# Kernel optimization log

Measured on AMD Instinct MI355X. Metric: run time of the kernel, lower is better.

The kernel has to match this reference:

```python
import math
import jax, jax.numpy as jnp
import numpy as np

THETA = 2 ** 16

def _get_freqs(n: int) -> jnp.ndarray:
    # positions quantized to multiples of 2 (pairs share a frequency)
    pos = jnp.floor(jnp.arange(n, dtype=jnp.float32) / 2.0) * 2.0
    return 1.0 / (THETA ** (pos / n)) / (2.0 * math.pi)  # (n,)

def _rope(phases: jnp.ndarray, v: jnp.ndarray) -> jnp.ndarray:
    # phases in 'cycles'; wrap to [0,1) then scale to radians
    ph = (phases % 1.0) * (2.0 * math.pi)
    c, s = jnp.cos(ph), jnp.sin(ph)
    # interleaved rotate-half: out[..., 2i] = -v[..., 2i+1], out[..., 2i+1] = v[..., 2i]
    v_rot = jnp.stack((-v[..., 1::2], v[..., ::2]), axis=-1).reshape(v.shape)
    return (v * c).astype(v.dtype) + (v_rot * s).astype(v.dtype)


def setup_inputs() -> dict:
    key = jax.random.key(0)
    kq, kv = jax.random.split(key)
    B, H, T, N, D = 2, 8, 2048, 1024, 128
    Q = jax.random.normal(kq, (B, H, T, N), dtype=jnp.float32)
    K = Q  # module asserts K is Q
    V = jax.random.normal(kv, (B, H, T, D), dtype=jnp.float32)
    return {"Q": Q, "K": K, "V": V}


def reference(Q, K, V):
    B, H, T, N = Q.shape
    freqs = _get_freqs(N)  # (N,)
    # r_phases: (T, N) = position * freq (broadcast over B, H)
    r_phases = jnp.arange(T, dtype=jnp.float32)[:, None] * freqs[None, :]
    QR = _rope(r_phases, Q)  # (B,H,T,N); KR = QR since K is Q
    scores = jnp.einsum('bhtn,bhsn->bhts', QR, QR)  # (B,H,T,T)
    causal = jnp.tril(jnp.ones((T, T), dtype=bool), k=-1)  # strict lower triangle
    scores = jnp.where(causal, scores, 0.0)
    return jnp.einsum('bhts,bhsd->bhtd', scores, V)  # (B,H,T,D)
```

## Files before the change

kernel.cpp:

```cpp
#include <hip/hip_runtime.h>

typedef __bf16 bf16_t;
typedef bf16_t bf16x8 __attribute__((ext_vector_type(8)));
typedef float f32x4 __attribute__((ext_vector_type(4)));
typedef unsigned short u16;
typedef unsigned int u32;

#define T_DIM 2048
#define N_DIM 1024
#define D_DIM 128

__device__ __forceinline__ u16 f32_to_bf16(float f) {
    u32 u = __builtin_bit_cast(u32, f);
    u += 0x7FFFu + ((u >> 16) & 1u);
    return (u16)(u >> 16);
}
__device__ __forceinline__ float bf16_to_f32(u16 v) {
    u32 u = (u32)v << 16;
    return __builtin_bit_cast(float, u);
}

typedef __attribute__((address_space(1))) const u32 guint;
typedef __attribute__((address_space(3))) u32 luint;
__device__ __forceinline__ void stage16(const void* g, void* l) {
    __builtin_amdgcn_global_load_lds((guint*)g, (luint*)l, 16, 0, 0);
}

__global__ void rope_kernel(const float* __restrict__ Q, u16* __restrict__ QR) {
    const int g = blockIdx.x * 256 + threadIdx.x;
    const int base = g * 4;
    const int t  = (base >> 9) & (T_DIM - 1);
    const int p0 = base & 511;
    const float4 qa = ((const float4*)Q)[g * 2];
    const float4 qb = ((const float4*)Q)[g * 2 + 1];
    const float vin[4][2] = {{qa.x, qa.y}, {qa.z, qa.w}, {qb.x, qb.y}, {qb.z, qb.w}};
    u16 ov[8];
    #pragma unroll
    for (int uu = 0; uu < 4; ++uu) {
        const float freq = exp2f((float)(p0 + uu) * (-1.0f / 32.0f)) * 0.15915494309189535f;
        float ph = (float)t * freq;
        ph = ph - floorf(ph);
        const float s = __builtin_amdgcn_sinf(ph);
        const float c = __builtin_amdgcn_cosf(ph);
        ov[2 * uu]     = f32_to_bf16(vin[uu][0] * c - vin[uu][1] * s);
        ov[2 * uu + 1] = f32_to_bf16(vin[uu][1] * c + vin[uu][0] * s);
    }
    ((uint4*)QR)[g] = *(const uint4*)ov;
}

__global__ void vt_kernel(const float* __restrict__ V, u16* __restrict__ Vt) {
    __shared__ u16 tile[64][65];
    const int bh   = blockIdx.x >> 6;
    const int rem  = blockIdx.x & 63;
    const int t0 = (rem >> 1) * 64, d0 = (rem & 1) * 64;
    const float* src = V + ((size_t)bh * T_DIM + t0) * D_DIM + d0;
    #pragma unroll
    for (int k = 0; k < 16; ++k) {
        int linear = k * 256 + threadIdx.x;
        int r = linear >> 6, c = linear & 63;
        tile[r][c] = f32_to_bf16(src[(size_t)r * D_DIM + c]);
    }
    __syncthreads();
    u16* dst = Vt + ((size_t)bh * D_DIM + d0) * T_DIM + t0;
    #pragma unroll
    for (int k = 0; k < 16; ++k) {
        int linear = k * 256 + threadIdx.x;
        int dr = linear >> 6, tc = linear & 63;
        dst[(size_t)dr * T_DIM + tc] = tile[tc][dr];
    }
}

__global__ void qrt_kernel(const u16* __restrict__ QR, u16* __restrict__ QRt) {
    __shared__ u16 til[64][65];
    const int bh  = blockIdx.x >> 9;
    const int rem = blockIdx.x & 511;
    const int t0 = (rem >> 4) * 64, n0 = (rem & 15) * 64;
    const u16* src = QR + (size_t)bh * ((size_t)T_DIM * N_DIM) + (size_t)t0 * N_DIM + n0;
    #pragma unroll
    for (int k = 0; k < 2; ++k) {
        int linear = k * 256 + threadIdx.x;
        int r = linear >> 3, o = linear & 7;
        uint4 v = *(const uint4*)(src + (size_t)r * N_DIM + o * 8);
        u16 tmp[8]; *(uint4*)tmp = v;
        #pragma unroll
        for (int e = 0; e < 8; ++e) til[r][o * 8 + e] = tmp[e];
    }
    __syncthreads();
    u16* dst = QRt + (size_t)bh * ((size_t)N_DIM * T_DIM) + (size_t)n0 * T_DIM + t0;
    #pragma unroll
    for (int k = 0; k < 2; ++k) {
        int linear = k * 256 + threadIdx.x;
        int nl = linear >> 3, to = linear & 7;
        u16 tmp[8];
        #pragma unroll
        for (int e = 0; e < 8; ++e) tmp[e] = til[to * 8 + e][nl];
        *(uint4*)(dst + (size_t)nl * T_DIM + to * 8) = *(const uint4*)tmp;
    }
}

__global__ __launch_bounds__(256, 2)
void state_kernel(const u16* __restrict__ QRt, const u16* __restrict__ Vt,
                  u16* __restrict__ U) {
    __shared__ __align__(16) u16 Smem[16384];
    u16 (*As)[64] = (u16 (*)[64])Smem;
    u16 (*Bs)[64] = (u16 (*)[64])(Smem + 8192);

    const int ci = blockIdx.x >> 3;
    const int nt = blockIdx.x & 7;
    const int bh = ci >> 4;
    const int i  = ci & 15;

    const int tid  = threadIdx.x;
    const int w    = tid >> 6;
    const int wy   = w >> 1, wx = w & 1;
    const int lane = tid & 63;
    const int quad = lane >> 4;
    const int l15  = lane & 15;
    const int sw   = l15 & 7;
    const int srow = lane >> 3;
    const int scol = (lane & 7) ^ (srow & 7);

    const u16* Ap = Vt + (size_t)bh * ((size_t)D_DIM * T_DIM)
                       + (size_t)(w * 32 + srow) * T_DIM + i * 128 + scol * 8;
    const u16* Bp = QRt + (size_t)bh * ((size_t)N_DIM * T_DIM)
                        + (size_t)(nt * 128 + w * 32 + srow) * T_DIM + i * 128 + scol * 8;

    const f32x4 fz = {0.f, 0.f, 0.f, 0.f};
    f32x4 acc[4][4];
    #pragma unroll
    for (int mi = 0; mi < 4; ++mi)
        #pragma unroll
        for (int nj = 0; nj < 4; ++nj)
            acc[mi][nj] = fz;

    for (int kk = 0; kk < 128; kk += 64) {
        #pragma unroll
        for (int ii = 0; ii < 4; ++ii) {
            stage16(Ap + (size_t)ii * 8 * T_DIM + kk, &As[w * 32 + ii * 8][0]);
            stage16(Bp + (size_t)ii * 8 * T_DIM + kk, &Bs[w * 32 + ii * 8][0]);
        }
        __syncthreads();
        #pragma unroll
        for (int kc = 0; kc < 2; ++kc) {
            bf16x8 af[4], bfr[4];
            #pragma unroll
            for (int mi = 0; mi < 4; ++mi)
                af[mi] = *(const bf16x8*)((const char*)As + (wy * 64 + mi * 16 + l15) * 128 + (((kc * 4 + quad) ^ sw) << 4));
            #pragma unroll
            for (int nj = 0; nj < 4; ++nj)
                bfr[nj] = *(const bf16x8*)((const char*)Bs + (wx * 64 + nj * 16 + l15) * 128 + (((kc * 4 + quad) ^ sw) << 4));
            #pragma unroll
            for (int mi = 0; mi < 4; ++mi)
                #pragma unroll
                for (int nj = 0; nj < 4; ++nj)
                    acc[mi][nj] = __builtin_amdgcn_mfma_f32_16x16x32_bf16(af[mi], bfr[nj], acc[mi][nj], 0, 0, 0);
        }
        __syncthreads();
    }

    u16* ub = U + (size_t)ci * (128 * (size_t)N_DIM) + nt * 128;
    #pragma unroll
    for (int mi = 0; mi < 4; ++mi)
        #pragma unroll
        for (int nj = 0; nj < 4; ++nj)
            #pragma unroll
            for (int rr = 0; rr < 4; ++rr)
                ub[(size_t)(wy * 64 + mi * 16 + quad * 4 + rr) * N_DIM + wx * 64 + nj * 16 + l15]
                    = f32_to_bf16(acc[mi][nj][rr]);
}

__global__ void scan_kernel(u16* __restrict__ UP) {
    const int tg  = blockIdx.x * 256 + threadIdx.x;
    const int bh  = tg >> 14;
    const int rem = tg & 16383;
    u16* base = UP + ((size_t)bh * 16 * 128 + (rem >> 7)) * N_DIM + (size_t)(rem & 127) * 8;
    float s[8];
    #pragma unroll
    for (int e = 0; e < 8; ++e) s[e] = 0.f;
    #pragma unroll 1
    for (int i = 0; i < 16; ++i) {
        u16* p = base + (size_t)i * (128 * (size_t)N_DIM);
        uint4 v = *(const uint4*)p;
        u16 in[8]; *(uint4*)in = v;
        u16 out[8];
        #pragma unroll
        for (int e = 0; e < 8; ++e) {
            float f = bf16_to_f32(in[e]);
            out[e]  = f32_to_bf16(s[e]);
            s[e]   += f;
        }
        *(uint4*)p = *(const uint4*)out;
    }
}

__global__ __launch_bounds__(256, 2)
void attn2_kernel(const u16* __restrict__ QR, const u16* __restrict__ Pt,
                  const u16* __restrict__ Vt, float* __restrict__ Out,
                  float* __restrict__ Part) {
    __shared__ __align__(16) u16 Smem[17920];
    u16 (*As)[64]  = (u16 (*)[64])Smem;
    u16 (*Bs)[64]  = (u16 (*)[64])(Smem + 8192);
    u16 (*Ps)[140] = (u16 (*)[140])Smem;

    const int b = blockIdx.x;
    const bool is_main = b < 256;
    const int ci = is_main ? b : b - 256;
    const int bh = ci >> 4;
    const int i  = ci & 15;

    const int tid  = threadIdx.x;
    const int w    = tid >> 6;
    const int wy   = w >> 1, wx = w & 1;
    const int lane = tid & 63;
    const int quad = lane >> 4;
    const int l15  = lane & 15;
    const int sw   = l15 & 7;
    const int srow = lane >> 3;
    const int scol = (lane & 7) ^ (srow & 7);

    const u16* QRb = QR + (size_t)bh * ((size_t)T_DIM * N_DIM);
    const u16* Ap  = QRb + (size_t)(i * 128 + w * 32 + srow) * N_DIM + scol * 8;
    const u16* Bp  = is_main
        ? Pt + (size_t)(ci * 128 + w * 32 + srow) * N_DIM + scol * 8
        : Ap;

    const f32x4 fz = {0.f, 0.f, 0.f, 0.f};
    f32x4 s_acc[4][4];
    #pragma unroll
    for (int mi = 0; mi < 4; ++mi)
        #pragma unroll
        for (int nj = 0; nj < 4; ++nj)
            s_acc[mi][nj] = fz;

    for (int kk = 0; kk < N_DIM; kk += 64) {
        #pragma unroll
        for (int ii = 0; ii < 4; ++ii) {
            stage16(Ap + (size_t)ii * 8 * N_DIM + kk, &As[w * 32 + ii * 8][0]);
            stage16(Bp + (size_t)ii * 8 * N_DIM + kk, &Bs[w * 32 + ii * 8][0]);
        }
        __syncthreads();
        #pragma unroll
        for (int kc = 0; kc < 2; ++kc) {
            bf16x8 af[4], bfr[4];
            #pragma unroll
            for (int mi = 0; mi < 4; ++mi)
                af[mi] = *(const bf16x8*)((const char*)As + (wy * 64 + mi * 16 + l15) * 128 + (((kc * 4 + quad) ^ sw) << 4));
            #pragma unroll
            for (int nj = 0; nj < 4; ++nj)
                bfr[nj] = *(const bf16x8*)((const char*)Bs + (wx * 64 + nj * 16 + l15) * 128 + (((kc * 4 + quad) ^ sw) << 4));
            #pragma unroll
            for (int mi = 0; mi < 4; ++mi)
                #pragma unroll
                for (int nj = 0; nj < 4; ++nj)
                    s_acc[mi][nj] = __builtin_amdgcn_mfma_f32_16x16x32_bf16(af[mi], bfr[nj], s_acc[mi][nj], 0, 0, 0);
        }
        __syncthreads();
    }

    if (is_main) {
        float* pb = Part + (size_t)ci * 16384;
        #pragma unroll
        for (int mi = 0; mi < 4; ++mi)
            #pragma unroll
            for (int nj = 0; nj < 4; ++nj)
                #pragma unroll
                for (int rr = 0; rr < 4; ++rr)
                    pb[(wy * 64 + mi * 16 + quad * 4 + rr) * 128 + wx * 64 + nj * 16 + l15]
                        = s_acc[mi][nj][rr];
    } else {
        #pragma unroll
        for (int mi = 0; mi < 4; ++mi) {
            const int rowb = wy * 64 + mi * 16 + quad * 4;
            #pragma unroll
            for (int nj = 0; nj < 4; ++nj) {
                const int col = wx * 64 + nj * 16 + l15;
                #pragma unroll
                for (int rr = 0; rr < 4; ++rr)
                    if (col >= rowb + rr) s_acc[mi][nj][rr] = 0.f;
            }
        }
        #pragma unroll
        for (int mi = 0; mi < 4; ++mi) {
            const int rowb = wy * 64 + mi * 16 + quad * 4;
            #pragma unroll
            for (int nj = 0; nj < 4; ++nj) {
                const int col = wx * 64 + nj * 16 + l15;
                #pragma unroll
                for (int rr = 0; rr < 4; ++rr)
                    Ps[rowb + rr][col] = f32_to_bf16(s_acc[mi][nj][rr]);
            }
        }
        __syncthreads();

        f32x4 o_acc[4][4];
        #pragma unroll
        for (int mi = 0; mi < 4; ++mi)
            #pragma unroll
            for (int nj = 0; nj < 4; ++nj)
                o_acc[mi][nj] = fz;

        const u16* vjb = Vt + (size_t)bh * ((size_t)D_DIM * T_DIM)
                            + (size_t)(wx * 64 + l15) * T_DIM + i * 128 + quad * 8;
        #pragma unroll
        for (int kc = 0; kc < 4; ++kc) {
            bf16x8 pf[4];
            #pragma unroll
            for (int mi = 0; mi < 4; ++mi)
                pf[mi] = *(const bf16x8*)(&Ps[wy * 64 + mi * 16 + l15][kc * 32 + quad * 8]);
            #pragma unroll
            for (int nj = 0; nj < 4; ++nj) {
                const bf16x8 vv = *(const bf16x8*)(vjb + (size_t)(nj * 16) * T_DIM + kc * 32);
                #pragma unroll
                for (int mi = 0; mi < 4; ++mi)
                    o_acc[mi][nj] = __builtin_amdgcn_mfma_f32_16x16x32_bf16(pf[mi], vv, o_acc[mi][nj], 0, 0, 0);
            }
        }

        float* ob = Out + ((size_t)bh * T_DIM + (size_t)i * 128) * D_DIM;
        #pragma unroll
        for (int mi = 0; mi < 4; ++mi)
            #pragma unroll
            for (int nj = 0; nj < 4; ++nj)
                #pragma unroll
                for (int rr = 0; rr < 4; ++rr)
                    ob[(size_t)(wy * 64 + mi * 16 + quad * 4 + rr) * D_DIM + wx * 64 + nj * 16 + l15]
                        = o_acc[mi][nj][rr];
    }
}

__global__ void combine2_kernel(float* __restrict__ Out, const float* __restrict__ Part) {
    const int idx = blockIdx.x * 256 + threadIdx.x;
    float4 a = ((float4*)Out)[idx];
    const float4 p = ((const float4*)Part)[idx];
    a.x += p.x; a.y += p.y; a.z += p.z; a.w += p.w;
    ((float4*)Out)[idx] = a;
}

__device__ __forceinline__ int run_start(int b) { return b < 128 ? 5 * b : 640 + 4 * (b - 128); }

__global__ __launch_bounds__(256, 2)
void attn_kernel(const u16* __restrict__ QR, const u16* __restrict__ Vt,
                 float* __restrict__ Out, u16* __restrict__ Part) {
    __shared__ __align__(16) u16 Smem[17920];
    u16 (*As)[64]  = (u16 (*)[64])Smem;
    u16 (*Bs)[64]  = (u16 (*)[64])(Smem + 8192);
    u16 (*Ps)[140] = (u16 (*)[140])Smem;

    const int b     = blockIdx.x;
    const int start = run_start(b);
    const int len   = b < 128 ? 5 : 4;

    const int tid  = threadIdx.x;
    const int w    = tid >> 6;
    const int wy   = w >> 1, wx = w & 1;
    const int lane = tid & 63;
    const int quad = lane >> 4;
    const int l15  = lane & 15;
    const int sw   = l15 & 7;
    const int srow = lane >> 3;
    const int scol = (lane & 7) ^ (srow & 7);

    const f32x4 fz = {0.f, 0.f, 0.f, 0.f};
    f32x4 o_acc[4][4];
    int cur_bh = -1, cur_qt = -1;
    bool hasj0 = false;
    const u16* QRb = QR;
    const u16* Ap  = QR;
    const u16* Vb  = Vt;

    for (int it = 0; it < len; ++it) {
        const int i = start + it;
        const int bh = i / 136;
        const int r  = i - bh * 136;
        int qt = 15, j = 0, acc = 0;
        #pragma unroll 1
        for (int q = 0; q < 16; ++q) {
            if (r < acc + q + 1) { qt = q; j = r - acc; break; }
            acc += q + 1;
        }

        if (qt != cur_qt || bh != cur_bh) {
            if (cur_qt >= 0) {
                if (hasj0) {
                    float* ob = Out + ((size_t)cur_bh * T_DIM + (size_t)cur_qt * 128) * D_DIM;
                    #pragma unroll
                    for (int mi = 0; mi < 4; ++mi)
                        #pragma unroll
                        for (int nj = 0; nj < 4; ++nj)
                            #pragma unroll
                            for (int rr = 0; rr < 4; ++rr)
                                ob[(size_t)(wy * 64 + mi * 16 + quad * 4 + rr) * D_DIM + wx * 64 + nj * 16 + l15] = o_acc[mi][nj][rr];
                } else {
                    u16* pb = Part + (size_t)b * 16384;
                    #pragma unroll
                    for (int mi = 0; mi < 4; ++mi)
                        #pragma unroll
                        for (int nj = 0; nj < 4; ++nj)
                            #pragma unroll
                            for (int rr = 0; rr < 4; ++rr)
                                pb[(wy * 64 + mi * 16 + quad * 4 + rr) * 128 + wx * 64 + nj * 16 + l15] = f32_to_bf16(o_acc[mi][nj][rr]);
                }
            }
            cur_bh = bh; cur_qt = qt; hasj0 = (j == 0);
            #pragma unroll
            for (int mi = 0; mi < 4; ++mi)
                #pragma unroll
                for (int nj = 0; nj < 4; ++nj)
                    o_acc[mi][nj] = fz;
            QRb = QR + (size_t)bh * (T_DIM * N_DIM);
            Ap  = QRb + (size_t)(qt * 128 + w * 32 + srow) * N_DIM + scol * 8;
            Vb  = Vt + (size_t)bh * (D_DIM * T_DIM) + (size_t)(wx * 64 + l15) * T_DIM + quad * 8;
        }

        const u16* Bp = QRb + (size_t)(j * 128 + w * 32 + srow) * N_DIM + scol * 8;
        f32x4 s_acc[4][4];
        #pragma unroll
        for (int mi = 0; mi < 4; ++mi)
            #pragma unroll
            for (int nj = 0; nj < 4; ++nj)
                s_acc[mi][nj] = fz;

        __syncthreads();

        for (int kk = 0; kk < N_DIM; kk += 64) {
            #pragma unroll
            for (int ii = 0; ii < 4; ++ii) {
                stage16(Ap + (size_t)ii * 8 * N_DIM + kk, &As[w * 32 + ii * 8][0]);
                stage16(Bp + (size_t)ii * 8 * N_DIM + kk, &Bs[w * 32 + ii * 8][0]);
            }
            __syncthreads();
            #pragma unroll
            for (int kc = 0; kc < 2; ++kc) {
                bf16x8 af[4], bfr[4];
                #pragma unroll
                for (int mi = 0; mi < 4; ++mi)
                    af[mi] = *(const bf16x8*)((const char*)As + (wy * 64 + mi * 16 + l15) * 128 + (((kc * 4 + quad) ^ sw) << 4));
                #pragma unroll
                for (int nj = 0; nj < 4; ++nj)
                    bfr[nj] = *(const bf16x8*)((const char*)Bs + (wx * 64 + nj * 16 + l15) * 128 + (((kc * 4 + quad) ^ sw) << 4));
                #pragma unroll
                for (int mi = 0; mi < 4; ++mi)
                    #pragma unroll
                    for (int nj = 0; nj < 4; ++nj)
                        s_acc[mi][nj] = __builtin_amdgcn_mfma_f32_16x16x32_bf16(af[mi], bfr[nj], s_acc[mi][nj], 0, 0, 0);
            }
            __syncthreads();
        }

        if (j == qt) {
            #pragma unroll
            for (int mi = 0; mi < 4; ++mi) {
                const int rowb = wy * 64 + mi * 16 + quad * 4;
                #pragma unroll
                for (int nj = 0; nj < 4; ++nj) {
                    const int col = wx * 64 + nj * 16 + l15;
                    #pragma unroll
                    for (int rr = 0; rr < 4; ++rr)
                        if (col >= rowb + rr) s_acc[mi][nj][rr] = 0.f;
                }
            }
        }

        #pragma unroll
        for (int mi = 0; mi < 4; ++mi) {
            const int rowb = wy * 64 + mi * 16 + quad * 4;
            #pragma unroll
            for (int nj = 0; nj < 4; ++nj) {
                const int col = wx * 64 + nj * 16 + l15;
                #pragma unroll
                for (int rr = 0; rr < 4; ++rr)
                    Ps[rowb + rr][col] = f32_to_bf16(s_acc[mi][nj][rr]);
            }
        }
        __syncthreads();

        const u16* vjb = Vb + j * 128;
        #pragma unroll
        for (int kc = 0; kc < 4; ++kc) {
            bf16x8 pf[4];
            #pragma unroll
            for (int mi = 0; mi < 4; ++mi)
                pf[mi] = *(const bf16x8*)(&Ps[wy * 64 + mi * 16 + l15][kc * 32 + quad * 8]);
            #pragma unroll
            for (int nj = 0; nj < 4; ++nj) {
                const bf16x8 vv = *(const bf16x8*)(vjb + (size_t)(nj * 16) * T_DIM + kc * 32);
                #pragma unroll
                for (int mi = 0; mi < 4; ++mi)
                    o_acc[mi][nj] = __builtin_amdgcn_mfma_f32_16x16x32_bf16(pf[mi], vv, o_acc[mi][nj], 0, 0, 0);
            }
        }
    }

    if (hasj0) {
        float* ob = Out + ((size_t)cur_bh * T_DIM + (size_t)cur_qt * 128) * D_DIM;
        #pragma unroll
        for (int mi = 0; mi < 4; ++mi)
            #pragma unroll
            for (int nj = 0; nj < 4; ++nj)
                #pragma unroll
                for (int rr = 0; rr < 4; ++rr)
                    ob[(size_t)(wy * 64 + mi * 16 + quad * 4 + rr) * D_DIM + wx * 64 + nj * 16 + l15] = o_acc[mi][nj][rr];
    } else {
        u16* pb = Part + (size_t)b * 16384;
        #pragma unroll
        for (int mi = 0; mi < 4; ++mi)
            #pragma unroll
            for (int nj = 0; nj < 4; ++nj)
                #pragma unroll
                for (int rr = 0; rr < 4; ++rr)
                    pb[(wy * 64 + mi * 16 + quad * 4 + rr) * 128 + wx * 64 + nj * 16 + l15] = f32_to_bf16(o_acc[mi][nj][rr]);
    }
}

__global__ void combine_kernel(float* __restrict__ Out, const u16* __restrict__ Part) {
    const int bh = blockIdx.x & 15;
    const int qt = 1 + (blockIdx.x >> 4);
    const int ts = bh * 136 + (qt * (qt + 1)) / 2;
    const int lo = ts + 1, hi = ts + qt;
    int bmin = (lo <= 640) ? (lo + 4) / 5 : 128 + (lo - 640 + 3) / 4;
    int writers[4], nw = 0;
    for (int bb = bmin; bb < 512 && run_start(bb) <= hi && nw < 4; ++bb)
        writers[nw++] = bb;
    if (nw == 0) return;
    float* ob = Out + ((size_t)bh * T_DIM + (size_t)qt * 128) * D_DIM;
    const int tid = threadIdx.x;
    #pragma unroll 1
    for (int e = 0; e < 64; ++e) {
        const int idx = e * 256 + tid;
        float a = ob[idx];
        for (int k = 0; k < nw; ++k)
            a += bf16_to_f32(Part[(size_t)writers[k] * 16384 + idx]);
        ob[idx] = a;
    }
}

extern "C" void kernel_launch(void* const* d_in, const int* in_sizes, int n_in,
                              void* d_out, int out_size, void* d_ws, size_t ws_size,
                              hipStream_t stream) {
    const float* Q = (const float*)d_in[0];
    const float* V = (const float*)d_in[2];
    float* Out = (float*)d_out;

    const size_t QR_E = (size_t)16 * T_DIM * N_DIM;
    const size_t VT_E = (size_t)16 * D_DIM * T_DIM;
    const size_t P_E  = (size_t)256 * 128 * N_DIM;
    const size_t need = (QR_E * 2 + VT_E + P_E) * 2 + (size_t)256 * 16384 * 4;

    if (ws_size >= need) {
        u16* QRw  = (u16*)d_ws;
        u16* QRtw = QRw + QR_E;
        u16* Vtw  = QRtw + QR_E;
        u16* Ptw  = Vtw + VT_E;
        float* PartF = (float*)(Ptw + P_E);

        rope_kernel<<<dim3(16384), dim3(256), 0, stream>>>(Q, QRw);
        vt_kernel<<<dim3(1024), dim3(256), 0, stream>>>(V, Vtw);
        qrt_kernel<<<dim3(8192), dim3(256), 0, stream>>>(QRw, QRtw);
        state_kernel<<<dim3(2048), dim3(256), 0, stream>>>(QRtw, Vtw, Ptw);
        scan_kernel<<<dim3(1024), dim3(256), 0, stream>>>(Ptw);
        attn2_kernel<<<dim3(512), dim3(256), 0, stream>>>(QRw, Ptw, Vtw, Out, PartF);
        combine2_kernel<<<dim3(4096), dim3(256), 0, stream>>>(Out, PartF);
    } else {
        u16* QRw  = (u16*)d_ws;
        u16* Vtw  = QRw + QR_E;
        u16* Part = Vtw + VT_E;

        rope_kernel<<<dim3(16384), dim3(256), 0, stream>>>(Q, QRw);
        vt_kernel<<<dim3(1024), dim3(256), 0, stream>>>(V, Vtw);
        attn_kernel<<<dim3(512), dim3(256), 0, stream>>>(QRw, Vtw, Out, Part);
        combine_kernel<<<dim3(240), dim3(256), 0, stream>>>(Out, Part);
    }
}
```

Before: 373.9 us.

## Fuse rope with transpose, state with scan, and merge attention blocks

Rope and the QR transpose now happen in one kernel, which removes a full re-read of QR. The per-chunk state GEMM and the prefix scan become one kernel that keeps a running fp32 accumulator across T chunks with double-buffered LDS staging, so the separate scan pass and its read-modify-write are gone. The inter-chunk and intra-chunk score GEMMs are merged into one attention kernel that shares A tiles and adds the intra result into the same accumulator, which eliminates combine2 and the fp32 partial buffer. The cost is fewer blocks (256) at occupancy 1, and the serial state kernel runs a 30-step loop, which can hurt parallelism on a GPU with many CUs.

```diff
diff --git a/kernel.cpp b/kernel.cpp
--- a/kernel.cpp
+++ b/kernel.cpp
@@ -24,6 +24,290 @@
 typedef __attribute__((address_space(3))) u32 luint;
 __device__ __forceinline__ void stage16(const void* g, void* l) {
     __builtin_amdgcn_global_load_lds((guint*)g, (luint*)l, 16, 0, 0);
+}
+__device__ __forceinline__ void wait_vm0_barrier() {
+    asm volatile("s_waitcnt vmcnt(0)" ::: "memory");
+    __builtin_amdgcn_s_barrier();
+}
+
+__global__ void ropet_kernel(const float* __restrict__ Q, u16* __restrict__ QR,
+                             u16* __restrict__ QRt) {
+    __shared__ u16 til[64][65];
+    const int bh  = blockIdx.x >> 9;
+    const int rem = blockIdx.x & 511;
+    const int t0 = (rem >> 4) * 64, n0 = (rem & 15) * 64;
+    const float* src = Q + (size_t)bh * ((size_t)T_DIM * N_DIM) + (size_t)t0 * N_DIM + n0;
+    u16* qdst = QR + (size_t)bh * ((size_t)T_DIM * N_DIM) + (size_t)t0 * N_DIM + n0;
+    #pragma unroll
+    for (int k = 0; k < 4; ++k) {
+        const int linear = k * 256 + threadIdx.x;
+        const int r = linear >> 4;
+        const int f = linear & 15;
+        const float4 q = *(const float4*)(src + (size_t)r * N_DIM + f * 4);
+        const int t = t0 + r;
+        u16 o[4];
+        #pragma unroll
+        for (int pp = 0; pp < 2; ++pp) {
+            const int pidx = ((n0 + f * 4) >> 1) + pp;
+            const float freq = exp2f((float)pidx * (-1.0f / 32.0f)) * 0.15915494309189535f;
+            float ph = (float)t * freq;
+            ph -= floorf(ph);
+            const float s = __builtin_amdgcn_sinf(ph);
+            const float c = __builtin_amdgcn_cosf(ph);
+            const float a  = pp ? q.z : q.x;
+            const float b2 = pp ? q.w : q.y;
+            o[2 * pp]     = f32_to_bf16(a * c - b2 * s);
+            o[2 * pp + 1] = f32_to_bf16(b2 * c + a * s);
+        }
+        *(uint2*)(qdst + (size_t)r * N_DIM + f * 4) = *(const uint2*)o;
+        til[r][f * 4 + 0] = o[0]; til[r][f * 4 + 1] = o[1];
+        til[r][f * 4 + 2] = o[2]; til[r][f * 4 + 3] = o[3];
+    }
+    __syncthreads();
+    u16* tdst = QRt + (size_t)bh * ((size_t)N_DIM * T_DIM) + (size_t)n0 * T_DIM + t0;
+    #pragma unroll
+    for (int k = 0; k < 2; ++k) {
+        const int linear = k * 256 + threadIdx.x;
+        const int nl = linear >> 3, o = linear & 7;
+        u16 tmp[8];
+        #pragma unroll
+        for (int e = 0; e < 8; ++e) tmp[e] = til[o * 8 + e][nl];
+        *(uint4*)(tdst + (size_t)nl * T_DIM + o * 8) = *(const uint4*)tmp;
+    }
+}
+
+__global__ void vt_kernel(const float* __restrict__ V, u16* __restrict__ Vt) {
+    __shared__ u16 tile[64][65];
+    const int bh   = blockIdx.x >> 6;
+    const int rem  = blockIdx.x & 63;
+    const int t0 = (rem >> 1) * 64, d0 = (rem & 1) * 64;
+    const float* src = V + ((size_t)bh * T_DIM + t0) * D_DIM + d0;
+    #pragma unroll
+    for (int k = 0; k < 16; ++k) {
+        int linear = k * 256 + threadIdx.x;
+        int r = linear >> 6, c = linear & 63;
+        tile[r][c] = f32_to_bf16(src[(size_t)r * D_DIM + c]);
+    }
+    __syncthreads();
+    u16* dst = Vt + ((size_t)bh * D_DIM + d0) * T_DIM + t0;
+    #pragma unroll
+    for (int k = 0; k < 16; ++k) {
+        int linear = k * 256 + threadIdx.x;
+        int dr = linear >> 6, tc = linear & 63;
+        dst[(size_t)dr * T_DIM + tc] = tile[tc][dr];
+    }
+}
+
+__global__ __launch_bounds__(256, 1)
+void statescan_kernel(const u16* __restrict__ QRt, const u16* __restrict__ Vt,
+                      u16* __restrict__ UP) {
+    __shared__ __align__(16) u16 Smem[24576];
+
+    const int b  = blockIdx.x;
+    const int bh = b >> 4;
+    const int nt = (b >> 1) & 7;
+    const int dt = b & 1;
+
+    const int tid  = threadIdx.x;
+    const int w    = tid >> 6;
+    const int wy   = w >> 1, wx = w & 1;
+    const int lane = tid & 63;
+    const int quad = lane >> 4;
+    const int l15  = lane & 15;
+    const int sw   = l15 & 7;
+    const int srow = lane >> 3;
+    const int scol = (lane & 7) ^ (srow & 7);
+
+    const u16* Ag = Vt  + (size_t)bh * ((size_t)D_DIM * T_DIM) + (size_t)(dt * 64)  * T_DIM;
+    const u16* Bg = QRt + (size_t)bh * ((size_t)N_DIM * T_DIM) + (size_t)(nt * 128) * T_DIM;
+
+    const f32x4 fz = {0.f, 0.f, 0.f, 0.f};
+    f32x4 acc[2][4];
+    #pragma unroll
+    for (int mi = 0; mi < 2; ++mi)
+        #pragma unroll
+        for (int nj = 0; nj < 4; ++nj)
+            acc[mi][nj] = fz;
+
+    auto STAGE = [&](int buf, int s) {
+        const int toff = s * 64;
+        #pragma unroll
+        for (int ia = 0; ia < 2; ++ia)
+            stage16(Ag + (size_t)(w * 16 + ia * 8 + srow) * T_DIM + toff + scol * 8,
+                    Smem + buf * 4096 + (w * 16 + ia * 8) * 64);
+        #pragma unroll
+        for (int ib = 0; ib < 4; ++ib)
+            stage16(Bg + (size_t)(w * 32 + ib * 8 + srow) * T_DIM + toff + scol * 8,
+                    Smem + 8192 + buf * 8192 + (w * 32 + ib * 8) * 64);
+    };
+
+    u16* upb = UP + (size_t)(bh * 16) * (128 * (size_t)N_DIM)
+                  + (size_t)(dt * 64) * N_DIM + nt * 128;
+
+    auto WRITE_UP = [&](int ci) {
+        u16* ub = upb + (size_t)ci * (128 * (size_t)N_DIM);
+        #pragma unroll
+        for (int mi = 0; mi < 2; ++mi)
+            #pragma unroll
+            for (int nj = 0; nj < 4; ++nj)
+                #pragma unroll
+                for (int rr = 0; rr < 4; ++rr)
+                    ub[(size_t)(wy * 32 + mi * 16 + quad * 4 + rr) * N_DIM + wx * 64 + nj * 16 + l15]
+                        = f32_to_bf16(acc[mi][nj][rr]);
+    };
+
+    STAGE(0, 0);
+    wait_vm0_barrier();
+    int buf = 0;
+    for (int s = 0; s < 30; ++s) {
+        if ((s & 1) == 0) WRITE_UP(s >> 1);
+        if (s < 29) STAGE(buf ^ 1, s + 1);
+        const char* As = (const char*)(Smem + buf * 4096);
+        const char* Bs = (const char*)(Smem + 8192 + buf * 8192);
+        #pragma unroll
+        for (int kc = 0; kc < 2; ++kc) {
+            bf16x8 af[2], bfr[4];
+            #pragma unroll
+            for (int mi = 0; mi < 2; ++mi)
+                af[mi] = *(const bf16x8*)(As + (wy * 32 + mi * 16 + l15) * 128 + (((kc * 4 + quad) ^ sw) << 4));
+            #pragma unroll
+            for (int nj = 0; nj < 4; ++nj)
+                bfr[nj] = *(const bf16x8*)(Bs + (wx * 64 + nj * 16 + l15) * 128 + (((kc * 4 + quad) ^ sw) << 4));
+            #pragma unroll
+            for (int mi = 0; mi < 2; ++mi)
+                #pragma unroll
+                for (int nj = 0; nj < 4; ++nj)
+                    acc[mi][nj] = __builtin_amdgcn_mfma_f32_16x16x32_bf16(af[mi], bfr[nj], acc[mi][nj], 0, 0, 0);
+        }
+        wait_vm0_barrier();
+        buf ^= 1;
+    }
+    WRITE_UP(15);
+}
+
+__global__ __launch_bounds__(256, 1)
+void attn3_kernel(const u16* __restrict__ QR, const u16* __restrict__ UP,
+                  const u16* __restrict__ Vt, float* __restrict__ Out) {
+    __shared__ __align__(16) u16 Smem[32768];
+    u16 (*Ps)[140] = (u16 (*)[140])Smem;
+
+    const int b  = blockIdx.x;
+    const int bh = b >> 4;
+    const int i  = b & 15;
+
+    const int tid  = threadIdx.x;
+    const int w    = tid >> 6;
+    const int wy   = w >> 1, wx = w & 1;
+    const int lane = tid & 63;
+    const int quad = lane >> 4;
+    const int l15  = lane & 15;
+    const int sw   = l15 & 7;
+    const int srow = lane >> 3;
+    const int scol = (lane & 7) ^ (srow & 7);
+
+    const u16* Ap = QR + (size_t)bh * ((size_t)T_DIM * N_DIM)
+                       + (size_t)(i * 128 + w * 32 + srow) * N_DIM + scol * 8;
+    const u16* Bp = UP + (size_t)(b * 128 + w * 32 + srow) * N_DIM + scol * 8;
+
+    const f32x4 fz = {0.f, 0.f, 0.f, 0.f};
+    f32x4 sm[4][4], si[4][4];
+    #pragma unroll
+    for (int mi = 0; mi < 4; ++mi)
+        #pragma unroll
+        for (int nj = 0; nj < 4; ++nj) {
+            sm[mi][nj] = fz;
+            si[mi][nj] = fz;
+        }
+
+    auto STAGE = [&](int buf, int kk16) {
+        const int kk = kk16 * 64;
+        #pragma unroll
+        for (int ii = 0; ii < 4; ++ii) {
+            stage16(Ap + (size_t)(ii * 8) * N_DIM + kk, Smem + buf * 8192 + (w * 32 + ii * 8) * 64);
+            stage16(Bp + (size_t)(ii * 8) * N_DIM + kk, Smem + 16384 + buf * 8192 + (w * 32 + ii * 8) * 64);
+        }
+    };
+
+    STAGE(0, 0);
+    wait_vm0_barrier();
+    int buf = 0;
+    for (int kk16 = 0; kk16 < 16; ++kk16) {
+        if (kk16 < 15) STAGE(buf ^ 1, kk16 + 1);
+        const char* As = (const char*)(Smem + buf * 8192);
+        const char* Bs = (const char*)(Smem + 16384 + buf * 8192);
+        #pragma unroll
+        for (int kc = 0; kc < 2; ++kc) {
+            bf16x8 af[4], bm[4], bi[4];
+            #pragma unroll
+            for (int mi = 0; mi < 4; ++mi)
+                af[mi] = *(const bf16x8*)(As + (wy * 64 + mi * 16 + l15) * 128 + (((kc * 4 + quad) ^ sw) << 4));
+            #pragma unroll
+            for (int nj = 0; nj < 4; ++nj) {
+                bm[nj] = *(const bf16x8*)(Bs + (wx * 64 + nj * 16 + l15) * 128 + (((kc * 4 + quad) ^ sw) << 4));
+                bi[nj] = *(const bf16x8*)(As + (wx * 64 + nj * 16 + l15) * 128 + (((kc * 4 + quad) ^ sw) << 4));
+            }
+            #pragma unroll
+            for (int mi = 0; mi < 4; ++mi)
+                #pragma unroll
+                for (int nj = 0; nj < 4; ++nj) {
+                    sm[mi][nj] = __builtin_amdgcn_mfma_f32_16x16x32_bf16(af[mi], bm[nj], sm[mi][nj], 0, 0, 0);
+                    si[mi][nj] = __builtin_amdgcn_mfma_f32_16x16x32_bf16(af[mi], bi[nj], si[mi][nj], 0, 0, 0);
+                }
+        }
+        wait_vm0_barrier();
+        buf ^= 1;
+    }
+
+    #pragma unroll
+    for (int mi = 0; mi < 4; ++mi) {
+        const int rowb = wy * 64 + mi * 16 + quad * 4;
+        #pragma unroll
+        for (int nj = 0; nj < 4; ++nj) {
+            const int col = wx * 64 + nj * 16 + l15;
+            #pragma unroll
+            for (int rr = 0; rr < 4; ++rr)
+                if (col >= rowb + rr) si[mi][nj][rr] = 0.f;
+        }
+    }
+    #pragma unroll
+    for (int mi = 0; mi < 4; ++mi) {
+        const int rowb = wy * 64 + mi * 16 + quad * 4;
+        #pragma unroll
+        for (int nj = 0; nj < 4; ++nj) {
+            const int col = wx * 64 + nj * 16 + l15;
+            #pragma unroll
+            for (int rr = 0; rr < 4; ++rr)
+                Ps[rowb + rr][col] = f32_to_bf16(si[mi][nj][rr]);
+        }
+    }
+    __syncthreads();
+
+    const u16* vjb = Vt + (size_t)bh * ((size_t)D_DIM * T_DIM)
+                        + (size_t)(wx * 64 + l15) * T_DIM + i * 128 + quad * 8;
+    #pragma unroll
+    for (int kc = 0; kc < 4; ++kc) {
+        bf16x8 pf[4];
+        #pragma unroll
+        for (int mi = 0; mi < 4; ++mi)
+            pf[mi] = *(const bf16x8*)(&Ps[wy * 64 + mi * 16 + l15][kc * 32 + quad * 8]);
+        #pragma unroll
+        for (int nj = 0; nj < 4; ++nj) {
+            const bf16x8 vv = *(const bf16x8*)(vjb + (size_t)(nj * 16) * T_DIM + kc * 32);
+            #pragma unroll
+            for (int mi = 0; mi < 4; ++mi)
+                sm[mi][nj] = __builtin_amdgcn_mfma_f32_16x16x32_bf16(pf[mi], vv, sm[mi][nj], 0, 0, 0);
+        }
+    }
+
+    float* ob = Out + ((size_t)bh * T_DIM + (size_t)i * 128) * D_DIM;
+    #pragma unroll
+    for (int mi = 0; mi < 4; ++mi)
+        #pragma unroll
+        for (int nj = 0; nj < 4; ++nj)
+            #pragma unroll
+            for (int rr = 0; rr < 4; ++rr)
+                ob[(size_t)(wy * 64 + mi * 16 + quad * 4 + rr) * D_DIM + wx * 64 + nj * 16 + l15]
+                    = sm[mi][nj][rr];
 }
 
 __global__ void rope_kernel(const float* __restrict__ Q, u16* __restrict__ QR) {
@@ -46,294 +330,6 @@
         ov[2 * uu + 1] = f32_to_bf16(vin[uu][1] * c + vin[uu][0] * s);
     }
     ((uint4*)QR)[g] = *(const uint4*)ov;
-}
-
-__global__ void vt_kernel(const float* __restrict__ V, u16* __restrict__ Vt) {
-    __shared__ u16 tile[64][65];
-    const int bh   = blockIdx.x >> 6;
-    const int rem  = blockIdx.x & 63;
-    const int t0 = (rem >> 1) * 64, d0 = (rem & 1) * 64;
-    const float* src = V + ((size_t)bh * T_DIM + t0) * D_DIM + d0;
-    #pragma unroll
-    for (int k = 0; k < 16; ++k) {
-        int linear = k * 256 + threadIdx.x;
-        int r = linear >> 6, c = linear & 63;
-        tile[r][c] = f32_to_bf16(src[(size_t)r * D_DIM + c]);
-    }
-    __syncthreads();
-    u16* dst = Vt + ((size_t)bh * D_DIM + d0) * T_DIM + t0;
-    #pragma unroll
-    for (int k = 0; k < 16; ++k) {
-        int linear = k * 256 + threadIdx.x;
-        int dr = linear >> 6, tc = linear & 63;
-        dst[(size_t)dr * T_DIM + tc] = tile[tc][dr];
-    }
-}
-
-__global__ void qrt_kernel(const u16* __restrict__ QR, u16* __restrict__ QRt) {
-    __shared__ u16 til[64][65];
-    const int bh  = blockIdx.x >> 9;
-    const int rem = blockIdx.x & 511;
-    const int t0 = (rem >> 4) * 64, n0 = (rem & 15) * 64;
-    const u16* src = QR + (size_t)bh * ((size_t)T_DIM * N_DIM) + (size_t)t0 * N_DIM + n0;
-    #pragma unroll
-    for (int k = 0; k < 2; ++k) {
-        int linear = k * 256 + threadIdx.x;
-        int r = linear >> 3, o = linear & 7;
-        uint4 v = *(const uint4*)(src + (size_t)r * N_DIM + o * 8);
-        u16 tmp[8]; *(uint4*)tmp = v;
-        #pragma unroll
-        for (int e = 0; e < 8; ++e) til[r][o * 8 + e] = tmp[e];
-    }
-    __syncthreads();
-    u16* dst = QRt + (size_t)bh * ((size_t)N_DIM * T_DIM) + (size_t)n0 * T_DIM + t0;
-    #pragma unroll
-    for (int k = 0; k < 2; ++k) {
-        int linear = k * 256 + threadIdx.x;
-        int nl = linear >> 3, to = linear & 7;
-        u16 tmp[8];
-        #pragma unroll
-        for (int e = 0; e < 8; ++e) tmp[e] = til[to * 8 + e][nl];
-        *(uint4*)(dst + (size_t)nl * T_DIM + to * 8) = *(const uint4*)tmp;
-    }
-}
-
-__global__ __launch_bounds__(256, 2)
-void state_kernel(const u16* __restrict__ QRt, const u16* __restrict__ Vt,
-                  u16* __restrict__ U) {
-    __shared__ __align__(16) u16 Smem[16384];
-    u16 (*As)[64] = (u16 (*)[64])Smem;
-    u16 (*Bs)[64] = (u16 (*)[64])(Smem + 8192);
-
-    const int ci = blockIdx.x >> 3;
-    const int nt = blockIdx.x & 7;
-    const int bh = ci >> 4;
-    const int i  = ci & 15;
-
-    const int tid  = threadIdx.x;
-    const int w    = tid >> 6;
-    const int wy   = w >> 1, wx = w & 1;
-    const int lane = tid & 63;
-    const int quad = lane >> 4;
-    const int l15  = lane & 15;
-    const int sw   = l15 & 7;
-    const int srow = lane >> 3;
-    const int scol = (lane & 7) ^ (srow & 7);
-
-    const u16* Ap = Vt + (size_t)bh * ((size_t)D_DIM * T_DIM)
-                       + (size_t)(w * 32 + srow) * T_DIM + i * 128 + scol * 8;
-    const u16* Bp = QRt + (size_t)bh * ((size_t)N_DIM * T_DIM)
-                        + (size_t)(nt * 128 + w * 32 + srow) * T_DIM + i * 128 + scol * 8;
-
-    const f32x4 fz = {0.f, 0.f, 0.f, 0.f};
-    f32x4 acc[4][4];
-    #pragma unroll
-    for (int mi = 0; mi < 4; ++mi)
-        #pragma unroll
-        for (int nj = 0; nj < 4; ++nj)
-            acc[mi][nj] = fz;
-
-    for (int kk = 0; kk < 128; kk += 64) {
-        #pragma unroll
-        for (int ii = 0; ii < 4; ++ii) {
-            stage16(Ap + (size_t)ii * 8 * T_DIM + kk, &As[w * 32 + ii * 8][0]);
-            stage16(Bp + (size_t)ii * 8 * T_DIM + kk, &Bs[w * 32 + ii * 8][0]);
-        }
-        __syncthreads();
-        #pragma unroll
-        for (int kc = 0; kc < 2; ++kc) {
-            bf16x8 af[4], bfr[4];
-            #pragma unroll
-            for (int mi = 0; mi < 4; ++mi)
-                af[mi] = *(const bf16x8*)((const char*)As + (wy * 64 + mi * 16 + l15) * 128 + (((kc * 4 + quad) ^ sw) << 4));
-            #pragma unroll
-            for (int nj = 0; nj < 4; ++nj)
-                bfr[nj] = *(const bf16x8*)((const char*)Bs + (wx * 64 + nj * 16 + l15) * 128 + (((kc * 4 + quad) ^ sw) << 4));
-            #pragma unroll
-            for (int mi = 0; mi < 4; ++mi)
-                #pragma unroll
-                for (int nj = 0; nj < 4; ++nj)
-                    acc[mi][nj] = __builtin_amdgcn_mfma_f32_16x16x32_bf16(af[mi], bfr[nj], acc[mi][nj], 0, 0, 0);
-        }
-        __syncthreads();
-    }
-
-    u16* ub = U + (size_t)ci * (128 * (size_t)N_DIM) + nt * 128;
-    #pragma unroll
-    for (int mi = 0; mi < 4; ++mi)
-        #pragma unroll
-        for (int nj = 0; nj < 4; ++nj)
-            #pragma unroll
-            for (int rr = 0; rr < 4; ++rr)
-                ub[(size_t)(wy * 64 + mi * 16 + quad * 4 + rr) * N_DIM + wx * 64 + nj * 16 + l15]
-                    = f32_to_bf16(acc[mi][nj][rr]);
-}
-
-__global__ void scan_kernel(u16* __restrict__ UP) {
-    const int tg  = blockIdx.x * 256 + threadIdx.x;
-    const int bh  = tg >> 14;
-    const int rem = tg & 16383;
-    u16* base = UP + ((size_t)bh * 16 * 128 + (rem >> 7)) * N_DIM + (size_t)(rem & 127) * 8;
-    float s[8];
-    #pragma unroll
-    for (int e = 0; e < 8; ++e) s[e] = 0.f;
-    #pragma unroll 1
-    for (int i = 0; i < 16; ++i) {
-        u16* p = base + (size_t)i * (128 * (size_t)N_DIM);
-        uint4 v = *(const uint4*)p;
-        u16 in[8]; *(uint4*)in = v;
-        u16 out[8];
-        #pragma unroll
-        for (int e = 0; e < 8; ++e) {
-            float f = bf16_to_f32(in[e]);
-            out[e]  = f32_to_bf16(s[e]);
-            s[e]   += f;
-        }
-        *(uint4*)p = *(const uint4*)out;
-    }
-}
-
-__global__ __launch_bounds__(256, 2)
-void attn2_kernel(const u16* __restrict__ QR, const u16* __restrict__ Pt,
-                  const u16* __restrict__ Vt, float* __restrict__ Out,
-                  float* __restrict__ Part) {
-    __shared__ __align__(16) u16 Smem[17920];
-    u16 (*As)[64]  = (u16 (*)[64])Smem;
-    u16 (*Bs)[64]  = (u16 (*)[64])(Smem + 8192);
-    u16 (*Ps)[140] = (u16 (*)[140])Smem;
-
-    const int b = blockIdx.x;
-    const bool is_main = b < 256;
-    const int ci = is_main ? b : b - 256;
-    const int bh = ci >> 4;
-    const int i  = ci & 15;
-
-    const int tid  = threadIdx.x;
-    const int w    = tid >> 6;
-    const int wy   = w >> 1, wx = w & 1;
-    const int lane = tid & 63;
-    const int quad = lane >> 4;
-    const int l15  = lane & 15;
-    const int sw   = l15 & 7;
-    const int srow = lane >> 3;
-    const int scol = (lane & 7) ^ (srow & 7);
-
-    const u16* QRb = QR + (size_t)bh * ((size_t)T_DIM * N_DIM);
-    const u16* Ap  = QRb + (size_t)(i * 128 + w * 32 + srow) * N_DIM + scol * 8;
-    const u16* Bp  = is_main
-        ? Pt + (size_t)(ci * 128 + w * 32 + srow) * N_DIM + scol * 8
-        : Ap;
-
-    const f32x4 fz = {0.f, 0.f, 0.f, 0.f};
-    f32x4 s_acc[4][4];
-    #pragma unroll
-    for (int mi = 0; mi < 4; ++mi)
-        #pragma unroll
-        for (int nj = 0; nj < 4; ++nj)
-            s_acc[mi][nj] = fz;
-
-    for (int kk = 0; kk < N_DIM; kk += 64) {
-        #pragma unroll
-        for (int ii = 0; ii < 4; ++ii) {
-            stage16(Ap + (size_t)ii * 8 * N_DIM + kk, &As[w * 32 + ii * 8][0]);
-            stage16(Bp + (size_t)ii * 8 * N_DIM + kk, &Bs[w * 32 + ii * 8][0]);
-        }
-        __syncthreads();
-        #pragma unroll
-        for (int kc = 0; kc < 2; ++kc) {
-            bf16x8 af[4], bfr[4];
-            #pragma unroll
-            for (int mi = 0; mi < 4; ++mi)
-                af[mi] = *(const bf16x8*)((const char*)As + (wy * 64 + mi * 16 + l15) * 128 + (((kc * 4 + quad) ^ sw) << 4));
-            #pragma unroll
-            for (int nj = 0; nj < 4; ++nj)
-                bfr[nj] = *(const bf16x8*)((const char*)Bs + (wx * 64 + nj * 16 + l15) * 128 + (((kc * 4 + quad) ^ sw) << 4));
-            #pragma unroll
-            for (int mi = 0; mi < 4; ++mi)
-                #pragma unroll
-                for (int nj = 0; nj < 4; ++nj)
-                    s_acc[mi][nj] = __builtin_amdgcn_mfma_f32_16x16x32_bf16(af[mi], bfr[nj], s_acc[mi][nj], 0, 0, 0);
-        }
-        __syncthreads();
-    }
-
-    if (is_main) {
-        float* pb = Part + (size_t)ci * 16384;
-        #pragma unroll
-        for (int mi = 0; mi < 4; ++mi)
-            #pragma unroll
-            for (int nj = 0; nj < 4; ++nj)
-                #pragma unroll
-                for (int rr = 0; rr < 4; ++rr)
-                    pb[(wy * 64 + mi * 16 + quad * 4 + rr) * 128 + wx * 64 + nj * 16 + l15]
-                        = s_acc[mi][nj][rr];
-    } else {
-        #pragma unroll
-        for (int mi = 0; mi < 4; ++mi) {
-            const int rowb = wy * 64 + mi * 16 + quad * 4;
-            #pragma unroll
-            for (int nj = 0; nj < 4; ++nj) {
-                const int col = wx * 64 + nj * 16 + l15;
-                #pragma unroll
-                for (int rr = 0; rr < 4; ++rr)
-                    if (col >= rowb + rr) s_acc[mi][nj][rr] = 0.f;
-            }
-        }
-        #pragma unroll
-        for (int mi = 0; mi < 4; ++mi) {
-            const int rowb = wy * 64 + mi * 16 + quad * 4;
-            #pragma unroll
-            for (int nj = 0; nj < 4; ++nj) {
-                const int col = wx * 64 + nj * 16 + l15;
-                #pragma unroll
-                for (int rr = 0; rr < 4; ++rr)
-                    Ps[rowb + rr][col] = f32_to_bf16(s_acc[mi][nj][rr]);
-            }
-        }
-        __syncthreads();
-
-        f32x4 o_acc[4][4];
-        #pragma unroll
-        for (int mi = 0; mi < 4; ++mi)
-            #pragma unroll
-            for (int nj = 0; nj < 4; ++nj)
-                o_acc[mi][nj] = fz;
-
-        const u16* vjb = Vt + (size_t)bh * ((size_t)D_DIM * T_DIM)
-                            + (size_t)(wx * 64 + l15) * T_DIM + i * 128 + quad * 8;
-        #pragma unroll
-        for (int kc = 0; kc < 4; ++kc) {
-            bf16x8 pf[4];
-            #pragma unroll
-            for (int mi = 0; mi < 4; ++mi)
-                pf[mi] = *(const bf16x8*)(&Ps[wy * 64 + mi * 16 + l15][kc * 32 + quad * 8]);
-            #pragma unroll
-            for (int nj = 0; nj < 4; ++nj) {
-                const bf16x8 vv = *(const bf16x8*)(vjb + (size_t)(nj * 16) * T_DIM + kc * 32);
-                #pragma unroll
-                for (int mi = 0; mi < 4; ++mi)
-                    o_acc[mi][nj] = __builtin_amdgcn_mfma_f32_16x16x32_bf16(pf[mi], vv, o_acc[mi][nj], 0, 0, 0);
-            }
-        }
-
-        float* ob = Out + ((size_t)bh * T_DIM + (size_t)i * 128) * D_DIM;
-        #pragma unroll
-        for (int mi = 0; mi < 4; ++mi)
-            #pragma unroll
-            for (int nj = 0; nj < 4; ++nj)
-                #pragma unroll
-                for (int rr = 0; rr < 4; ++rr)
-                    ob[(size_t)(wy * 64 + mi * 16 + quad * 4 + rr) * D_DIM + wx * 64 + nj * 16 + l15]
-                        = o_acc[mi][nj][rr];
-    }
-}
-
-__global__ void combine2_kernel(float* __restrict__ Out, const float* __restrict__ Part) {
-    const int idx = blockIdx.x * 256 + threadIdx.x;
-    float4 a = ((float4*)Out)[idx];
-    const float4 p = ((const float4*)Part)[idx];
-    a.x += p.x; a.y += p.y; a.z += p.z; a.w += p.w;
-    ((float4*)Out)[idx] = a;
 }
 
 __device__ __forceinline__ int run_start(int b) { return b < 128 ? 5 * b : 640 + 4 * (b - 128); }
@@ -543,23 +539,19 @@
 
     const size_t QR_E = (size_t)16 * T_DIM * N_DIM;
     const size_t VT_E = (size_t)16 * D_DIM * T_DIM;
-    const size_t P_E  = (size_t)256 * 128 * N_DIM;
-    const size_t need = (QR_E * 2 + VT_E + P_E) * 2 + (size_t)256 * 16384 * 4;
+    const size_t UP_E = (size_t)256 * 128 * N_DIM;
+    const size_t need = (QR_E * 2 + VT_E + UP_E) * 2;
 
     if (ws_size >= need) {
         u16* QRw  = (u16*)d_ws;
         u16* QRtw = QRw + QR_E;
         u16* Vtw  = QRtw + QR_E;
-        u16* Ptw  = Vtw + VT_E;
-        float* PartF = (float*)(Ptw + P_E);
-
-        rope_kernel<<<dim3(16384), dim3(256), 0, stream>>>(Q, QRw);
+        u16* UPw  = Vtw + VT_E;
+
+        ropet_kernel<<<dim3(8192), dim3(256), 0, stream>>>(Q, QRw, QRtw);
         vt_kernel<<<dim3(1024), dim3(256), 0, stream>>>(V, Vtw);
-        qrt_kernel<<<dim3(8192), dim3(256), 0, stream>>>(QRw, QRtw);
-        state_kernel<<<dim3(2048), dim3(256), 0, stream>>>(QRtw, Vtw, Ptw);
-        scan_kernel<<<dim3(1024), dim3(256), 0, stream>>>(Ptw);
-        attn2_kernel<<<dim3(512), dim3(256), 0, stream>>>(QRw, Ptw, Vtw, Out, PartF);
-        combine2_kernel<<<dim3(4096), dim3(256), 0, stream>>>(Out, PartF);
+        statescan_kernel<<<dim3(256), dim3(256), 0, stream>>>(QRtw, Vtw, UPw);
+        attn3_kernel<<<dim3(256), dim3(256), 0, stream>>>(QRw, UPw, Vtw, Out);
     } else {
         u16* QRw  = (u16*)d_ws;
         u16* Vtw  = QRw + QR_E;
```

New measurement: 365.1 us. 2.4% less time.
